# Optimization experiments

Measured on AMD Instinct MI355X. Metric: run time of the kernel, lower is better.

Reference implementation:

```python
import jax, jax.numpy as jnp
import numpy as np

B, S, D = 2, 2048, 1024
H, HD = 16, 64
MLP = 4096
EPS = 1e-5


def layer_norm(x, g, b):
    mu = jnp.mean(x, axis=-1, keepdims=True)
    var = jnp.mean(jnp.square(x - mu), axis=-1, keepdims=True)
    return (x - mu) * jax.lax.rsqrt(var + EPS) * g + b


def setup_inputs() -> dict:
    key = jax.random.key(0)
    ks = jax.random.split(key, 12)
    s = 0.02
    return {
        "x": jax.random.normal(ks[0], (B, S, D), jnp.float32),
        "ln1_g": jnp.ones((D,), jnp.float32),
        "ln1_b": jnp.zeros((D,), jnp.float32),
        "Wq": jax.random.normal(ks[1], (D, H * HD), jnp.float32) * s,
        "Wk": jax.random.normal(ks[2], (D, H * HD), jnp.float32) * s,
        "Wv": jax.random.normal(ks[3], (D, H * HD), jnp.float32) * s,
        "Wo": jax.random.normal(ks[4], (H * HD, D), jnp.float32) * s,
        "ln2_g": jnp.ones((D,), jnp.float32),
        "ln2_b": jnp.zeros((D,), jnp.float32),
        "fc1_w": jax.random.normal(ks[5], (D, MLP), jnp.float32) * s,
        "fc1_b": jnp.zeros((MLP,), jnp.float32),
        "fc2_w": jax.random.normal(ks[6], (MLP, D), jnp.float32) * s,
        "fc2_b": jnp.zeros((D,), jnp.float32),
    }


def reference(x, ln1_g, ln1_b, Wq, Wk, Wv, Wo, ln2_g, ln2_b, fc1_w, fc1_b, fc2_w, fc2_b):
    b, s, d = x.shape
    scale = 1.0 / np.sqrt(HD)
    h = layer_norm(x, ln1_g, ln1_b)
    # project and split heads: [b, H, s, HD]
    q = (h @ Wq).reshape(b, s, H, HD).transpose(0, 2, 1, 3)
    k = (h @ Wk).reshape(b, s, H, HD).transpose(0, 2, 1, 3)
    v = (h @ Wv).reshape(b, s, H, HD).transpose(0, 2, 1, 3)
    scores = jnp.einsum('bhqd,bhkd->bhqk', q, k) * scale
    causal = jnp.where(jnp.tril(jnp.ones((s, s), bool)), 0.0, -jnp.inf).astype(x.dtype)
    scores = scores + causal[None, None]
    attn_weights = jax.nn.softmax(scores, axis=-1)
    attn_out = jnp.einsum('bhqk,bhkd->bhqd', attn_weights, v)
    attn_out = attn_out.transpose(0, 2, 1, 3).reshape(b, s, H * HD) @ Wo
    x = x + attn_out
    h2 = layer_norm(x, ln2_g, ln2_b)
    mlp = jax.nn.gelu(h2 @ fc1_w + fc1_b, approximate=True) @ fc2_w + fc2_b
    x = x + mlp
    return (x, attn_weights)
```

## Files before the change

### kernel.cpp

```cpp
#include <hip/hip_runtime.h>
#include <cmath>

typedef __bf16 bf16;
typedef __bf16 bf16x8 __attribute__((ext_vector_type(8)));
typedef float f32x4 __attribute__((ext_vector_type(4)));

#define B_ 2
#define S_ 2048
#define D_ 1024
#define H_ 16
#define HD_ 64
#define MLP_ 4096
#define XOUT_ ((size_t)B_ * S_ * D_)

#define SBAR() __builtin_amdgcn_s_barrier()
#define VMCNT(N) asm volatile("s_waitcnt vmcnt(" #N ")" ::: "memory")
#define SFENCE() asm volatile("" ::: "memory")

__device__ __forceinline__ void gll16(const void* g, void* l) {
  __builtin_amdgcn_global_load_lds((const __attribute__((address_space(1))) void*)g,
                                   (__attribute__((address_space(3))) void*)l, 16, 0, 0);
}

__device__ __forceinline__ f32x4 mfma16(bf16x8 a, bf16x8 b, f32x4 c) {
  return __builtin_amdgcn_mfma_f32_16x16x32_bf16(a, b, c, 0, 0, 0);
}

__device__ __forceinline__ float bfu2f(unsigned short u) {
  return __uint_as_float(((unsigned int)u) << 16);
}
__device__ __forceinline__ unsigned short f2bu(float v) {
  union { bf16 b; unsigned short u; } c; c.b = (bf16)v; return c.u;
}
__device__ __forceinline__ float ld_sc(const void* p, size_t i, int f32) {
  return f32 ? ((const float*)p)[i] : bfu2f(((const unsigned short*)p)[i]);
}

__device__ __forceinline__ int swz(int row, int col) {
  int byo = row * 128 + col * 2;
  return (byo ^ (((byo >> 9) & 3) << 5)) >> 1;
}

__global__ __launch_bounds__(64) void detect_k(const unsigned short* __restrict__ x,
                                               int* __restrict__ flag) {
  int tid = threadIdx.x;
  int cnt = 0;
  for (int i = tid; i < 512; i += 64) {
    int e = (x[i] >> 7) & 0xFF;
    if (e >= 0xBF) cnt++;
  }
  #pragma unroll
  for (int d = 1; d < 64; d <<= 1) cnt += __shfl_xor(cnt, d);
  if (tid == 0) flag[0] = (cnt > 8) ? 1 : 0;
}

__global__ __launch_bounds__(256) void transpose_ad(const void* __restrict__ in,
                                                    unsigned short* __restrict__ out,
                                                    int R, int C,
                                                    const int* __restrict__ flagp) {
  __shared__ unsigned short t[64][68];
  const int f32 = flagp[0];
  const int tid = threadIdx.x;
  const int c0 = blockIdx.x * 64, r0 = blockIdx.y * 64;
  for (int i = tid * 4; i < 4096; i += 1024) {
    int rr = i >> 6, cc = i & 63;
    size_t off = (size_t)(r0 + rr) * C + c0 + cc;
    if (f32) {
      float4 f = *(const float4*)((const float*)in + off);
      t[rr][cc + 0] = f2bu(f.x); t[rr][cc + 1] = f2bu(f.y);
      t[rr][cc + 2] = f2bu(f.z); t[rr][cc + 3] = f2bu(f.w);
    } else {
      *(ushort4*)&t[rr][cc] = *(const ushort4*)((const unsigned short*)in + off);
    }
  }
  __syncthreads();
  for (int i = tid * 4; i < 4096; i += 1024) {
    int orr = i & 63, oc = i >> 6;
    ushort4 v;
    v.x = t[orr + 0][oc]; v.y = t[orr + 1][oc];
    v.z = t[orr + 2][oc]; v.w = t[orr + 3][oc];
    *(ushort4*)(out + (size_t)(c0 + oc) * R + r0 + orr) = v;
  }
}

__global__ __launch_bounds__(256) void vtrans_k(const unsigned short* __restrict__ qkv,
                                                unsigned short* __restrict__ vT) {
  __shared__ unsigned short t[64][68];
  const int tid = threadIdx.x;
  const int s0 = blockIdx.x * 64, h = blockIdx.y, b = blockIdx.z;
  for (int i = tid * 4; i < 4096; i += 1024) {
    int si = i >> 6, hd = i & 63;
    *(ushort4*)&t[si][hd] =
        *(const ushort4*)(qkv + (size_t)(b * S_ + s0 + si) * 3072 + 2048 + h * 64 + hd);
  }
  __syncthreads();
  for (int i = tid * 4; i < 4096; i += 1024) {
    int ss = i & 63, hd = i >> 6;
    ushort4 v;
    v.x = t[ss + 0][hd]; v.y = t[ss + 1][hd];
    v.z = t[ss + 2][hd]; v.w = t[ss + 3][hd];
    *(ushort4*)(vT + ((size_t)(b * H_ + h) * 64 + hd) * S_ + s0 + ss) = v;
  }
}

__global__ __launch_bounds__(256) void ln_k(const void* __restrict__ xv,
                                            const void* __restrict__ g,
                                            const void* __restrict__ bvec,
                                            bf16* __restrict__ out,
                                            const int* __restrict__ flagp,
                                            int force_xf32) {
  const int f32 = flagp[0];
  const int xf32 = force_xf32 ? 1 : f32;
  const int row = blockIdx.x, tid = threadIdx.x;
  float v[4];
  if (xf32) {
    float4 f = *(const float4*)((const float*)xv + (size_t)row * 1024 + tid * 4);
    v[0] = f.x; v[1] = f.y; v[2] = f.z; v[3] = f.w;
  } else {
    ushort4 u = *(const ushort4*)((const unsigned short*)xv + (size_t)row * 1024 + tid * 4);
    v[0] = bfu2f(u.x); v[1] = bfu2f(u.y); v[2] = bfu2f(u.z); v[3] = bfu2f(u.w);
  }
  float s = 0.f, q = 0.f;
  #pragma unroll
  for (int i = 0; i < 4; i++) { s += v[i]; q += v[i] * v[i]; }
  #pragma unroll
  for (int d = 1; d < 64; d <<= 1) { s += __shfl_xor(s, d); q += __shfl_xor(q, d); }
  __shared__ float red[8];
  if ((tid & 63) == 0) { red[(tid >> 6) * 2] = s; red[(tid >> 6) * 2 + 1] = q; }
  __syncthreads();
  s = red[0] + red[2] + red[4] + red[6];
  q = red[1] + red[3] + red[5] + red[7];
  const float mean = s * (1.0f / 1024.0f);
  const float var = q * (1.0f / 1024.0f) - mean * mean;
  const float rs = rsqrtf(var + 1e-5f);
  unsigned short ov[4];
  #pragma unroll
  for (int i = 0; i < 4; i++) {
    float gg = ld_sc(g, tid * 4 + i, f32);
    float bb = ld_sc(bvec, tid * 4 + i, f32);
    ov[i] = f2bu((v[i] - mean) * rs * gg + bb);
  }
  ushort4 o4; o4.x = ov[0]; o4.y = ov[1]; o4.z = ov[2]; o4.w = ov[3];
  *(ushort4*)((unsigned short*)out + (size_t)row * 1024 + tid * 4) = o4;
}

template <int MODE>
__global__ __launch_bounds__(256) void gemm_bt(const bf16* __restrict__ A,
                                               const bf16* __restrict__ BT,
                                               int N, int K,
                                               const void* __restrict__ bias,
                                               const void* __restrict__ resb,
                                               const float* __restrict__ resf,
                                               bf16* __restrict__ outb,
                                               float* __restrict__ outf,
                                               const int* __restrict__ flagp) {
  __shared__ __align__(16) bf16 sA[128 * 64];
  __shared__ __align__(16) bf16 sB[128 * 64];
  const int f32 = flagp[0];
  const int tid = threadIdx.x;
  const int lane = tid & 63;
  const int wave = tid >> 6;
  const int wm = wave >> 1, wn = wave & 1;
  const int m0 = blockIdx.y * 128, n0 = blockIdx.x * 128;
  const int cn = lane & 15, rl = lane >> 4;
  const int r0 = tid >> 3, c16 = tid & 7;

  f32x4 zero = {0.f, 0.f, 0.f, 0.f};
  f32x4 acc[4][4];
  #pragma unroll
  for (int i = 0; i < 4; i++)
    #pragma unroll
    for (int j = 0; j < 4; j++) acc[i][j] = zero;

  for (int k0 = 0; k0 < K; k0 += 64) {
    __syncthreads();
    #pragma unroll
    for (int i = 0; i < 4; i++) {
      int row = r0 + i * 32;
      gll16(A + (size_t)(m0 + row) * K + k0 + c16 * 8, &sA[row * 64 + c16 * 8]);
      gll16(BT + (size_t)(n0 + row) * K + k0 + c16 * 8, &sB[row * 64 + c16 * 8]);
    }
    __syncthreads();
    #pragma unroll
    for (int kk = 0; kk < 64; kk += 32) {
      bf16x8 af[4], bfr[4];
      #pragma unroll
      for (int t = 0; t < 4; t++) {
        af[t] = *(const bf16x8*)&sA[(wm * 64 + t * 16 + cn) * 64 + kk + rl * 8];
        bfr[t] = *(const bf16x8*)&sB[(wn * 64 + t * 16 + cn) * 64 + kk + rl * 8];
      }
      #pragma unroll
      for (int mt = 0; mt < 4; mt++)
        #pragma unroll
        for (int nt = 0; nt < 4; nt++)
          acc[mt][nt] = mfma16(af[mt], bfr[nt], acc[mt][nt]);
    }
  }

  #pragma unroll
  for (int mt = 0; mt < 4; mt++) {
    #pragma unroll
    for (int nt = 0; nt < 4; nt++) {
      #pragma unroll
      for (int j = 0; j < 4; j++) {
        const int row = m0 + wm * 64 + mt * 16 + rl * 4 + j;
        const int col = n0 + wn * 64 + nt * 16 + cn;
        const size_t idx = (size_t)row * N + col;
        float v = acc[mt][nt][j];
        if (MODE == 0) {
          outb[idx] = (bf16)v;
        } else if (MODE == 1) {
          v += ld_sc(bias, col, f32);
          float u = 0.7978845608028654f * (v + 0.044715f * v * v * v);
          float gl = v / (1.0f + exp2f(-2.8853900817779268f * u));
          outb[idx] = (bf16)gl;
        } else if (MODE == 2) {
          outf[idx] = v + ld_sc(resb, idx, f32);
        } else {
          float val = v + ld_sc(bias, col, f32) + resf[idx];
          if (f32) outf[idx] = val; else outb[idx] = (bf16)val;
        }
      }
    }
  }
}

__global__ __launch_bounds__(256) void attn_k(const bf16* __restrict__ qkv,
                                              const bf16* __restrict__ vT,
                                              void* __restrict__ Pv,
                                              bf16* __restrict__ ao,
                                              const int* __restrict__ flagp) {
  __shared__ __align__(16) bf16 sK[2][64 * 64];
  __shared__ __align__(16) bf16 sV[2][64 * 64];
  __shared__ __align__(16) bf16 sP[4][16 * 64];
  const int f32o = flagp[0];
  const int tid = threadIdx.x, lane = tid & 63, wave = tid >> 6;
  const int qt = (int)(gridDim.x - 1 - blockIdx.x);
  const int h = blockIdx.y, b = blockIdx.z;
  const float scale2 = 0.18033688011112042f;
  const float NEG = -1e30f;
  const int cn = lane & 15, rl = lane >> 4;

  int urow[2], ucol[2], ldst[2];
  #pragma unroll
  for (int i = 0; i < 2; i++) {
    int Lb = tid * 16 + i * 4096;
    int Ub = Lb ^ (((Lb >> 9) & 3) << 5);
    urow[i] = Ub >> 7;
    ucol[i] = (Ub & 127) >> 1;
    ldst[i] = Lb >> 1;
  }

  const bf16* kbase = qkv + (size_t)b * S_ * 3072 + 1024 + h * 64;
  const bf16* vbase = vT + ((size_t)(b * H_ + h) * 64) * S_;

  bf16x8 aq[2];
  {
    const bf16* qb = qkv + (size_t)(b * S_ + qt * 64 + wave * 16 + cn) * 3072 + h * 64;
    aq[0] = *(const bf16x8*)(qb + rl * 8);
    aq[1] = *(const bf16x8*)(qb + 32 + rl * 8);
  }

  #pragma unroll
  for (int i = 0; i < 2; i++)
    gll16(kbase + (size_t)urow[i] * 3072 + ucol[i], &sK[0][ldst[i]]);
  VMCNT(0);
  SBAR();

  float m_i[4], l_i[4];
  #pragma unroll
  for (int j = 0; j < 4; j++) { m_i[j] = NEG; l_i[j] = 0.0f; }

  int cur = 0;
  for (int kt = 0; kt <= qt; kt++) {
    if (kt < qt) {
      #pragma unroll
      for (int i = 0; i < 2; i++)
        gll16(kbase + (size_t)((kt + 1) * 64 + urow[i]) * 3072 + ucol[i], &sK[cur ^ 1][ldst[i]]);
      SFENCE();
    }
    f32x4 s[4];
    f32x4 zero = {0.f, 0.f, 0.f, 0.f};
    #pragma unroll
    for (int nt = 0; nt < 4; nt++) s[nt] = zero;
    #pragma unroll
    for (int kx = 0; kx < 2; kx++)
      #pragma unroll
      for (int nt = 0; nt < 4; nt++) {
        bf16x8 bb = *(const bf16x8*)&sK[cur][swz(nt * 16 + cn, kx * 32 + rl * 8)];
        s[nt] = mfma16(aq[kx], bb, s[nt]);
      }
    float pm[4] = {NEG, NEG, NEG, NEG};
    if (kt == qt) {
      #pragma unroll
      for (int nt = 0; nt < 4; nt++)
        #pragma unroll
        for (int j = 0; j < 4; j++) {
          float v = (nt * 16 + cn > wave * 16 + rl * 4 + j) ? NEG : s[nt][j] * scale2;
          s[nt][j] = v;
          pm[j] = fmaxf(pm[j], v);
        }
    } else {
      #pragma unroll
      for (int nt = 0; nt < 4; nt++)
        #pragma unroll
        for (int j = 0; j < 4; j++) {
          float v = s[nt][j] * scale2;
          s[nt][j] = v;
          pm[j] = fmaxf(pm[j], v);
        }
    }
    #pragma unroll
    for (int j = 0; j < 4; j++) {
      #pragma unroll
      for (int d = 1; d < 16; d <<= 1) pm[j] = fmaxf(pm[j], __shfl_xor(pm[j], d));
      float mn = fmaxf(m_i[j], pm[j]);
      float ps = exp2f(s[0][j] - mn) + exp2f(s[1][j] - mn) +
                 exp2f(s[2][j] - mn) + exp2f(s[3][j] - mn);
      #pragma unroll
      for (int d = 1; d < 16; d <<= 1) ps += __shfl_xor(ps, d);
      l_i[j] = l_i[j] * exp2f(m_i[j] - mn) + ps;
      m_i[j] = mn;
    }
    if (kt < qt) { VMCNT(0); SBAR(); cur ^= 1; }
  }

  float inv_l[4];
  #pragma unroll
  for (int j = 0; j < 4; j++) inv_l[j] = 1.0f / l_i[j];

  SBAR();
  #pragma unroll
  for (int i = 0; i < 2; i++) {
    gll16(kbase + (size_t)urow[i] * 3072 + ucol[i], &sK[0][ldst[i]]);
    gll16(vbase + (size_t)urow[i] * S_ + ucol[i], &sV[0][ldst[i]]);
  }
  VMCNT(0);
  SBAR();
  cur = 0;

  f32x4 o[4];
  {
    f32x4 zero = {0.f, 0.f, 0.f, 0.f};
    #pragma unroll
    for (int nt = 0; nt < 4; nt++) o[nt] = zero;
  }

  for (int kt = 0; kt <= qt; kt++) {
    if (kt < qt) {
      #pragma unroll
      for (int i = 0; i < 2; i++) {
        gll16(kbase + (size_t)((kt + 1) * 64 + urow[i]) * 3072 + ucol[i], &sK[cur ^ 1][ldst[i]]);
        gll16(vbase + (size_t)urow[i] * S_ + (kt + 1) * 64 + ucol[i], &sV[cur ^ 1][ldst[i]]);
      }
      SFENCE();
    }
    f32x4 s[4];
    f32x4 zero = {0.f, 0.f, 0.f, 0.f};
    #pragma unroll
    for (int nt = 0; nt < 4; nt++) s[nt] = zero;
    #pragma unroll
    for (int kx = 0; kx < 2; kx++)
      #pragma unroll
      for (int nt = 0; nt < 4; nt++) {
        bf16x8 bb = *(const bf16x8*)&sK[cur][swz(nt * 16 + cn, kx * 32 + rl * 8)];
        s[nt] = mfma16(aq[kx], bb, s[nt]);
      }
    if (kt == qt) {
      #pragma unroll
      for (int nt = 0; nt < 4; nt++)
        #pragma unroll
        for (int j = 0; j < 4; j++) {
          bool masked = (nt * 16 + cn > wave * 16 + rl * 4 + j);
          float p = masked ? 0.0f : exp2f(s[nt][j] * scale2 - m_i[j]) * inv_l[j];
          sP[wave][swz(rl * 4 + j, nt * 16 + cn)] = (bf16)p;
        }
    } else {
      #pragma unroll
      for (int nt = 0; nt < 4; nt++)
        #pragma unroll
        for (int j = 0; j < 4; j++) {
          float p = exp2f(s[nt][j] * scale2 - m_i[j]) * inv_l[j];
          sP[wave][swz(rl * 4 + j, nt * 16 + cn)] = (bf16)p;
        }
    }
    {
      size_t base = XOUT_ + (((size_t)b * H_ + h) * S_ + qt * 64 + wave * 16) * S_ + kt * 64;
      #pragma unroll
      for (int i = 0; i < 2; i++) {
        int idx = lane + i * 64;
        int r = idx >> 3, cc = idx & 7;
        uint4 val = *(const uint4*)&sP[wave][swz(r, cc * 8)];
        if (f32o) {
          float4 lo, hi;
          lo.x = __uint_as_float(val.x << 16); lo.y = __uint_as_float(val.x & 0xffff0000u);
          lo.z = __uint_as_float(val.y << 16); lo.w = __uint_as_float(val.y & 0xffff0000u);
          hi.x = __uint_as_float(val.z << 16); hi.y = __uint_as_float(val.z & 0xffff0000u);
          hi.z = __uint_as_float(val.w << 16); hi.w = __uint_as_float(val.w & 0xffff0000u);
          *(float4*)((float*)Pv + base + (size_t)r * S_ + cc * 8) = lo;
          *(float4*)((float*)Pv + base + (size_t)r * S_ + cc * 8 + 4) = hi;
        } else {
          *(uint4*)((bf16*)Pv + base + (size_t)r * S_ + cc * 8) = val;
        }
      }
    }
    #pragma unroll
    for (int kx = 0; kx < 2; kx++) {
      bf16x8 ap = *(const bf16x8*)&sP[wave][swz(cn, kx * 32 + rl * 8)];
      #pragma unroll
      for (int nt = 0; nt < 4; nt++) {
        bf16x8 bv = *(const bf16x8*)&sV[cur][swz(nt * 16 + cn, kx * 32 + rl * 8)];
        o[nt] = mfma16(ap, bv, o[nt]);
      }
    }
    if (kt < qt) {
      if (f32o) { VMCNT(4); } else { VMCNT(2); }
      SBAR();
      cur ^= 1;
    }
  }

  {
    const int t0 = qt + 1;
    const int nch = (32 - t0) * 8;
    size_t rowbase = XOUT_ + (((size_t)b * H_ + h) * S_ + qt * 64) * S_;
    uint4 z; z.x = 0; z.y = 0; z.z = 0; z.w = 0;
    for (int idx = tid; idx < 64 * nch; idx += 256) {
      int r = idx / nch, cc = idx % nch;
      size_t off = rowbase + (size_t)r * S_ + t0 * 64 + cc * 8;
      if (f32o) {
        *(uint4*)((float*)Pv + off) = z;
        *(uint4*)((float*)Pv + off + 4) = z;
      } else {
        *(uint4*)((bf16*)Pv + off) = z;
      }
    }
  }

  #pragma unroll
  for (int nt = 0; nt < 4; nt++)
    #pragma unroll
    for (int j = 0; j < 4; j++) {
      int rowg2 = b * S_ + qt * 64 + wave * 16 + rl * 4 + j;
      ao[(size_t)rowg2 * 1024 + h * 64 + nt * 16 + cn] = (bf16)o[nt][j];
    }
}

extern "C" void kernel_launch(void* const* d_in, const int* in_sizes, int n_in,
                              void* d_out, int out_size, void* d_ws, size_t ws_size,
                              hipStream_t stream) {
  (void)in_sizes; (void)n_in; (void)out_size; (void)ws_size;
  const void* x    = d_in[0];
  const void* ln1g = d_in[1];
  const void* ln1b = d_in[2];
  const void* Wq   = d_in[3];
  const void* Wk   = d_in[4];
  const void* Wv   = d_in[5];
  const void* Wo   = d_in[6];
  const void* ln2g = d_in[7];
  const void* ln2b = d_in[8];
  const void* fc1w = d_in[9];
  const void* fc1b = d_in[10];
  const void* fc2w = d_in[11];
  const void* fc2b = d_in[12];

  char* ws = (char*)d_ws;
  bf16* wqkvT = (bf16*)(ws + 0);
  bf16* woT   = (bf16*)(ws + 6291456);
  bf16* fc1T  = (bf16*)(ws + 8388608);
  bf16* fc2T  = (bf16*)(ws + 16777216);
  bf16* h     = (bf16*)(ws + 25165824);
  bf16* qkv   = (bf16*)(ws + 33554432);
  bf16* vT    = (bf16*)(ws + 58720256);
  bf16* m1    = (bf16*)(ws + 33554432);
  bf16* aout  = (bf16*)(ws + 67108864);
  float* x1   = (float*)(ws + 75497472);
  int* flag   = (int*)(ws + 92274688);

  dim3 blk(256);

  detect_k<<<1, 64, 0, stream>>>((const unsigned short*)x, flag);

  transpose_ad<<<dim3(16, 16), blk, 0, stream>>>(Wq, (unsigned short*)wqkvT, 1024, 1024, flag);
  transpose_ad<<<dim3(16, 16), blk, 0, stream>>>(Wk, (unsigned short*)(wqkvT + 1024 * 1024), 1024, 1024, flag);
  transpose_ad<<<dim3(16, 16), blk, 0, stream>>>(Wv, (unsigned short*)(wqkvT + 2 * 1024 * 1024), 1024, 1024, flag);
  transpose_ad<<<dim3(16, 16), blk, 0, stream>>>(Wo, (unsigned short*)woT, 1024, 1024, flag);
  transpose_ad<<<dim3(64, 16), blk, 0, stream>>>(fc1w, (unsigned short*)fc1T, 1024, 4096, flag);
  transpose_ad<<<dim3(16, 64), blk, 0, stream>>>(fc2w, (unsigned short*)fc2T, 4096, 1024, flag);

  ln_k<<<4096, blk, 0, stream>>>(x, ln1g, ln1b, h, flag, 0);

  gemm_bt<0><<<dim3(24, 32), blk, 0, stream>>>(h, wqkvT, 3072, 1024, nullptr, nullptr, nullptr, qkv, nullptr, flag);

  vtrans_k<<<dim3(32, 16, 2), blk, 0, stream>>>((const unsigned short*)qkv, (unsigned short*)vT);

  attn_k<<<dim3(32, 16, 2), blk, 0, stream>>>(qkv, vT, d_out, aout, flag);

  gemm_bt<2><<<dim3(8, 32), blk, 0, stream>>>(aout, woT, 1024, 1024, nullptr, x, nullptr, nullptr, x1, flag);

  ln_k<<<4096, blk, 0, stream>>>(x1, ln2g, ln2b, h, flag, 1);

  gemm_bt<1><<<dim3(32, 32), blk, 0, stream>>>(h, fc1T, 4096, 1024, fc1b, nullptr, nullptr, m1, nullptr, flag);

  gemm_bt<3><<<dim3(8, 32), blk, 0, stream>>>(m1, fc2T, 1024, 4096, fc2b, nullptr, x1, (bf16*)d_out, (float*)d_out, flag);
}
```

Baseline: 1.075 ms.

## Add 128x64 GEMM tiles, XCD-aware block remap, deeper attention prefetch, fused weight transposes

Merges the four square weight transposes into one launch. Adds a block-ID remap in the GEMMs and the attention kernel so that consecutive workgroups, which land on different XCDs, share tiles within each XCD's L2. Adds a 128x64-tile GEMM for the N=1024 output projection and fc2 so those launches have twice as many workgroups. In the attention statistics pass it prefetches K two tiles ahead and defers the cross-lane max/sum reductions to the end of the loop. This raises occupancy and cache locality but adds index arithmetic and reduces reuse per tile in the narrower GEMM.

```diff
diff --git a/kernel.cpp b/kernel.cpp
--- a/kernel.cpp
+++ b/kernel.cpp
@@ -83,6 +83,41 @@
   }
 }
 
+__global__ __launch_bounds__(256) void transpose4_ad(const void* __restrict__ i0,
+                                                     const void* __restrict__ i1,
+                                                     const void* __restrict__ i2,
+                                                     const void* __restrict__ i3,
+                                                     unsigned short* __restrict__ wqkvT,
+                                                     unsigned short* __restrict__ woT,
+                                                     const int* __restrict__ flagp) {
+  __shared__ unsigned short t[64][68];
+  const int f32 = flagp[0];
+  const int tid = threadIdx.x;
+  const int z = blockIdx.z;
+  const void* in = (z == 0) ? i0 : (z == 1) ? i1 : (z == 2) ? i2 : i3;
+  unsigned short* out = (z < 3) ? (wqkvT + (size_t)z * 1024 * 1024) : woT;
+  const int c0 = blockIdx.x * 64, r0 = blockIdx.y * 64;
+  for (int i = tid * 4; i < 4096; i += 1024) {
+    int rr = i >> 6, cc = i & 63;
+    size_t off = (size_t)(r0 + rr) * 1024 + c0 + cc;
+    if (f32) {
+      float4 f = *(const float4*)((const float*)in + off);
+      t[rr][cc + 0] = f2bu(f.x); t[rr][cc + 1] = f2bu(f.y);
+      t[rr][cc + 2] = f2bu(f.z); t[rr][cc + 3] = f2bu(f.w);
+    } else {
+      *(ushort4*)&t[rr][cc] = *(const ushort4*)((const unsigned short*)in + off);
+    }
+  }
+  __syncthreads();
+  for (int i = tid * 4; i < 4096; i += 1024) {
+    int orr = i & 63, oc = i >> 6;
+    ushort4 v;
+    v.x = t[orr + 0][oc]; v.y = t[orr + 1][oc];
+    v.z = t[orr + 2][oc]; v.w = t[orr + 3][oc];
+    *(ushort4*)(out + (size_t)(c0 + oc) * 1024 + r0 + orr) = v;
+  }
+}
+
 __global__ __launch_bounds__(256) void vtrans_k(const unsigned short* __restrict__ qkv,
                                                 unsigned short* __restrict__ vT) {
   __shared__ unsigned short t[64][68];
@@ -161,7 +196,10 @@
   const int lane = tid & 63;
   const int wave = tid >> 6;
   const int wm = wave >> 1, wn = wave & 1;
-  const int m0 = blockIdx.y * 128, n0 = blockIdx.x * 128;
+  const int nwg = gridDim.x * gridDim.y;
+  const int fid = blockIdx.y * gridDim.x + blockIdx.x;
+  const int wg = ((nwg & 7) == 0) ? ((fid & 7) * (nwg >> 3) + (fid >> 3)) : fid;
+  const int m0 = (wg / gridDim.x) * 128, n0 = (wg % gridDim.x) * 128;
   const int cn = lane & 15, rl = lane >> 4;
   const int r0 = tid >> 3, c16 = tid & 7;
 
@@ -225,18 +263,101 @@
   }
 }
 
+template <int MODE>
+__global__ __launch_bounds__(256) void gemm_n64(const bf16* __restrict__ A,
+                                                const bf16* __restrict__ BT,
+                                                int N, int K,
+                                                const void* __restrict__ bias,
+                                                const void* __restrict__ resb,
+                                                const float* __restrict__ resf,
+                                                bf16* __restrict__ outb,
+                                                float* __restrict__ outf,
+                                                const int* __restrict__ flagp) {
+  __shared__ __align__(16) bf16 sA[128 * 64];
+  __shared__ __align__(16) bf16 sB[64 * 64];
+  const int f32 = flagp[0];
+  const int tid = threadIdx.x;
+  const int lane = tid & 63;
+  const int wave = tid >> 6;
+  const int nwg = gridDim.x * gridDim.y;
+  const int fid = blockIdx.y * gridDim.x + blockIdx.x;
+  const int wg = ((nwg & 7) == 0) ? ((fid & 7) * (nwg >> 3) + (fid >> 3)) : fid;
+  const int m0 = (wg / gridDim.x) * 128, n0 = (wg % gridDim.x) * 64;
+  const int cn = lane & 15, rl = lane >> 4;
+  const int r0 = tid >> 3, c16 = tid & 7;
+
+  f32x4 zero = {0.f, 0.f, 0.f, 0.f};
+  f32x4 acc[2][4];
+  #pragma unroll
+  for (int i = 0; i < 2; i++)
+    #pragma unroll
+    for (int j = 0; j < 4; j++) acc[i][j] = zero;
+
+  for (int k0 = 0; k0 < K; k0 += 64) {
+    __syncthreads();
+    #pragma unroll
+    for (int i = 0; i < 4; i++) {
+      int row = r0 + i * 32;
+      gll16(A + (size_t)(m0 + row) * K + k0 + c16 * 8, &sA[row * 64 + c16 * 8]);
+    }
+    #pragma unroll
+    for (int i = 0; i < 2; i++) {
+      int row = r0 + i * 32;
+      gll16(BT + (size_t)(n0 + row) * K + k0 + c16 * 8, &sB[row * 64 + c16 * 8]);
+    }
+    __syncthreads();
+    #pragma unroll
+    for (int kk = 0; kk < 64; kk += 32) {
+      bf16x8 af[2], bfr[4];
+      #pragma unroll
+      for (int t = 0; t < 2; t++)
+        af[t] = *(const bf16x8*)&sA[(wave * 32 + t * 16 + cn) * 64 + kk + rl * 8];
+      #pragma unroll
+      for (int t = 0; t < 4; t++)
+        bfr[t] = *(const bf16x8*)&sB[(t * 16 + cn) * 64 + kk + rl * 8];
+      #pragma unroll
+      for (int mt = 0; mt < 2; mt++)
+        #pragma unroll
+        for (int nt = 0; nt < 4; nt++)
+          acc[mt][nt] = mfma16(af[mt], bfr[nt], acc[mt][nt]);
+    }
+  }
+
+  #pragma unroll
+  for (int mt = 0; mt < 2; mt++) {
+    #pragma unroll
+    for (int nt = 0; nt < 4; nt++) {
+      #pragma unroll
+      for (int j = 0; j < 4; j++) {
+        const int row = m0 + wave * 32 + mt * 16 + rl * 4 + j;
+        const int col = n0 + nt * 16 + cn;
+        const size_t idx = (size_t)row * N + col;
+        float v = acc[mt][nt][j];
+        if (MODE == 2) {
+          outf[idx] = v + ld_sc(resb, idx, f32);
+        } else {
+          float val = v + ld_sc(bias, col, f32) + resf[idx];
+          if (f32) outf[idx] = val; else outb[idx] = (bf16)val;
+        }
+      }
+    }
+  }
+}
+
 __global__ __launch_bounds__(256) void attn_k(const bf16* __restrict__ qkv,
                                               const bf16* __restrict__ vT,
                                               void* __restrict__ Pv,
                                               bf16* __restrict__ ao,
                                               const int* __restrict__ flagp) {
-  __shared__ __align__(16) bf16 sK[2][64 * 64];
-  __shared__ __align__(16) bf16 sV[2][64 * 64];
+  __shared__ __align__(16) bf16 sKV[4][64 * 64];
   __shared__ __align__(16) bf16 sP[4][16 * 64];
   const int f32o = flagp[0];
   const int tid = threadIdx.x, lane = tid & 63, wave = tid >> 6;
-  const int qt = (int)(gridDim.x - 1 - blockIdx.x);
-  const int h = blockIdx.y, b = blockIdx.z;
+  const int fid = blockIdx.x;
+  const int c8 = fid & 7, kk8 = fid >> 3;
+  const int qt = 31 - (kk8 & 31);
+  const int p = c8 + 8 * (kk8 >> 5);
+  const int h = p & 15, b = p >> 4;
   const float scale2 = 0.18033688011112042f;
   const float NEG = -1e30f;
   const int cn = lane & 15, rl = lane >> 4;
@@ -261,83 +382,84 @@
     aq[1] = *(const bf16x8*)(qb + 32 + rl * 8);
   }
 
-  #pragma unroll
-  for (int i = 0; i < 2; i++)
-    gll16(kbase + (size_t)urow[i] * 3072 + ucol[i], &sK[0][ldst[i]]);
+#define STAGEK(kt_, s_) { \
+    _Pragma("unroll") for (int i = 0; i < 2; i++) \
+      gll16(kbase + (size_t)((kt_) * 64 + urow[i]) * 3072 + ucol[i], &sKV[s_][ldst[i]]); }
+#define STAGEV(kt_, s_) { \
+    _Pragma("unroll") for (int i = 0; i < 2; i++) \
+      gll16(vbase + (size_t)urow[i] * S_ + (kt_) * 64 + ucol[i], &sKV[s_][ldst[i]]); }
+
+  float m_i[4], l_i[4];
+  #pragma unroll
+  for (int j = 0; j < 4; j++) { m_i[j] = NEG; l_i[j] = 0.0f; }
+
+  STAGEK(0, 0);
+  if (qt >= 1) { STAGEK(1, 1); SFENCE(); VMCNT(2); } else { VMCNT(0); }
+  SBAR();
+
+  for (int kt = 0; kt <= qt; kt++) {
+    if (kt + 2 <= qt) { STAGEK(kt + 2, ((kt + 2) & 3)); SFENCE(); }
+    const int slot = kt & 3;
+    f32x4 s4[4];
+    f32x4 zero = {0.f, 0.f, 0.f, 0.f};
+    #pragma unroll
+    for (int nt = 0; nt < 4; nt++) s4[nt] = zero;
+    #pragma unroll
+    for (int kx = 0; kx < 2; kx++)
+      #pragma unroll
+      for (int nt = 0; nt < 4; nt++) {
+        bf16x8 bb = *(const bf16x8*)&sKV[slot][swz(nt * 16 + cn, kx * 32 + rl * 8)];
+        s4[nt] = mfma16(aq[kx], bb, s4[nt]);
+      }
+    if (kt == qt) {
+      #pragma unroll
+      for (int nt = 0; nt < 4; nt++)
+        #pragma unroll
+        for (int j = 0; j < 4; j++)
+          s4[nt][j] = (nt * 16 + cn > wave * 16 + rl * 4 + j) ? NEG : s4[nt][j] * scale2;
+    } else {
+      #pragma unroll
+      for (int nt = 0; nt < 4; nt++)
+        #pragma unroll
+        for (int j = 0; j < 4; j++) s4[nt][j] *= scale2;
+    }
+    #pragma unroll
+    for (int j = 0; j < 4; j++) {
+      float pm = fmaxf(fmaxf(s4[0][j], s4[1][j]), fmaxf(s4[2][j], s4[3][j]));
+      float mn = fmaxf(m_i[j], pm);
+      float ps = exp2f(s4[0][j] - mn) + exp2f(s4[1][j] - mn) +
+                 exp2f(s4[2][j] - mn) + exp2f(s4[3][j] - mn);
+      l_i[j] = l_i[j] * exp2f(m_i[j] - mn) + ps;
+      m_i[j] = mn;
+    }
+    if (kt < qt) {
+      if (kt + 2 <= qt) { VMCNT(2); } else { VMCNT(0); }
+      SBAR();
+    }
+  }
+
+  #pragma unroll
+  for (int j = 0; j < 4; j++) {
+    float mr = m_i[j];
+    #pragma unroll
+    for (int d = 1; d < 16; d <<= 1) mr = fmaxf(mr, __shfl_xor(mr, d));
+    float lr = l_i[j] * exp2f(m_i[j] - mr);
+    #pragma unroll
+    for (int d = 1; d < 16; d <<= 1) lr += __shfl_xor(lr, d);
+    m_i[j] = mr;
+    l_i[j] = lr;
+  }
+
+  float inv_l[4];
+  #pragma unroll
+  for (int j = 0; j < 4; j++) inv_l[j] = 1.0f / l_i[j];
+
+  SBAR();
+  STAGEK(0, 0);
+  STAGEV(0, 2);
   VMCNT(0);
   SBAR();
-
-  float m_i[4], l_i[4];
-  #pragma unroll
-  for (int j = 0; j < 4; j++) { m_i[j] = NEG; l_i[j] = 0.0f; }
-
   int cur = 0;
-  for (int kt = 0; kt <= qt; kt++) {
-    if (kt < qt) {
-      #pragma unroll
-      for (int i = 0; i < 2; i++)
-        gll16(kbase + (size_t)((kt + 1) * 64 + urow[i]) * 3072 + ucol[i], &sK[cur ^ 1][ldst[i]]);
-      SFENCE();
-    }
-    f32x4 s[4];
-    f32x4 zero = {0.f, 0.f, 0.f, 0.f};
-    #pragma unroll
-    for (int nt = 0; nt < 4; nt++) s[nt] = zero;
-    #pragma unroll
-    for (int kx = 0; kx < 2; kx++)
-      #pragma unroll
-      for (int nt = 0; nt < 4; nt++) {
-        bf16x8 bb = *(const bf16x8*)&sK[cur][swz(nt * 16 + cn, kx * 32 + rl * 8)];
-        s[nt] = mfma16(aq[kx], bb, s[nt]);
-      }
-    float pm[4] = {NEG, NEG, NEG, NEG};
-    if (kt == qt) {
-      #pragma unroll
-      for (int nt = 0; nt < 4; nt++)
-        #pragma unroll
-        for (int j = 0; j < 4; j++) {
-          float v = (nt * 16 + cn > wave * 16 + rl * 4 + j) ? NEG : s[nt][j] * scale2;
-          s[nt][j] = v;
-          pm[j] = fmaxf(pm[j], v);
-        }
-    } else {
-      #pragma unroll
-      for (int nt = 0; nt < 4; nt++)
-        #pragma unroll
-        for (int j = 0; j < 4; j++) {
-          float v = s[nt][j] * scale2;
-          s[nt][j] = v;
-          pm[j] = fmaxf(pm[j], v);
-        }
-    }
-    #pragma unroll
-    for (int j = 0; j < 4; j++) {
-      #pragma unroll
-      for (int d = 1; d < 16; d <<= 1) pm[j] = fmaxf(pm[j], __shfl_xor(pm[j], d));
-      float mn = fmaxf(m_i[j], pm[j]);
-      float ps = exp2f(s[0][j] - mn) + exp2f(s[1][j] - mn) +
-                 exp2f(s[2][j] - mn) + exp2f(s[3][j] - mn);
-      #pragma unroll
-      for (int d = 1; d < 16; d <<= 1) ps += __shfl_xor(ps, d);
-      l_i[j] = l_i[j] * exp2f(m_i[j] - mn) + ps;
-      m_i[j] = mn;
-    }
-    if (kt < qt) { VMCNT(0); SBAR(); cur ^= 1; }
-  }
-
-  float inv_l[4];
-  #pragma unroll
-  for (int j = 0; j < 4; j++) inv_l[j] = 1.0f / l_i[j];
-
-  SBAR();
-  #pragma unroll
-  for (int i = 0; i < 2; i++) {
-    gll16(kbase + (size_t)urow[i] * 3072 + ucol[i], &sK[0][ldst[i]]);
-    gll16(vbase + (size_t)urow[i] * S_ + ucol[i], &sV[0][ldst[i]]);
-  }
-  VMCNT(0);
-  SBAR();
-  cur = 0;
 
   f32x4 o[4];
   {
@@ -348,23 +470,20 @@
 
   for (int kt = 0; kt <= qt; kt++) {
     if (kt < qt) {
-      #pragma unroll
-      for (int i = 0; i < 2; i++) {
-        gll16(kbase + (size_t)((kt + 1) * 64 + urow[i]) * 3072 + ucol[i], &sK[cur ^ 1][ldst[i]]);
-        gll16(vbase + (size_t)urow[i] * S_ + (kt + 1) * 64 + ucol[i], &sV[cur ^ 1][ldst[i]]);
-      }
+      STAGEK(kt + 1, (cur ^ 1));
+      STAGEV(kt + 1, (2 + (cur ^ 1)));
       SFENCE();
     }
-    f32x4 s[4];
+    f32x4 s4[4];
     f32x4 zero = {0.f, 0.f, 0.f, 0.f};
     #pragma unroll
-    for (int nt = 0; nt < 4; nt++) s[nt] = zero;
+    for (int nt = 0; nt < 4; nt++) s4[nt] = zero;
     #pragma unroll
     for (int kx = 0; kx < 2; kx++)
       #pragma unroll
       for (int nt = 0; nt < 4; nt++) {
-        bf16x8 bb = *(const bf16x8*)&sK[cur][swz(nt * 16 + cn, kx * 32 + rl * 8)];
-        s[nt] = mfma16(aq[kx], bb, s[nt]);
+        bf16x8 bb = *(const bf16x8*)&sKV[cur][swz(nt * 16 + cn, kx * 32 + rl * 8)];
+        s4[nt] = mfma16(aq[kx], bb, s4[nt]);
       }
     if (kt == qt) {
       #pragma unroll
@@ -372,16 +491,16 @@
         #pragma unroll
         for (int j = 0; j < 4; j++) {
           bool masked = (nt * 16 + cn > wave * 16 + rl * 4 + j);
-          float p = masked ? 0.0f : exp2f(s[nt][j] * scale2 - m_i[j]) * inv_l[j];
-          sP[wave][swz(rl * 4 + j, nt * 16 + cn)] = (bf16)p;
+          float pv = masked ? 0.0f : exp2f(s4[nt][j] * scale2 - m_i[j]) * inv_l[j];
+          sP[wave][swz(rl * 4 + j, nt * 16 + cn)] = (bf16)pv;
         }
     } else {
       #pragma unroll
       for (int nt = 0; nt < 4; nt++)
         #pragma unroll
         for (int j = 0; j < 4; j++) {
-          float p = exp2f(s[nt][j] * scale2 - m_i[j]) * inv_l[j];
-          sP[wave][swz(rl * 4 + j, nt * 16 + cn)] = (bf16)p;
+          float pv = exp2f(s4[nt][j] * scale2 - m_i[j]) * inv_l[j];
+          sP[wave][swz(rl * 4 + j, nt * 16 + cn)] = (bf16)pv;
         }
     }
     {
@@ -409,7 +528,7 @@
       bf16x8 ap = *(const bf16x8*)&sP[wave][swz(cn, kx * 32 + rl * 8)];
       #pragma unroll
       for (int nt = 0; nt < 4; nt++) {
-        bf16x8 bv = *(const bf16x8*)&sV[cur][swz(nt * 16 + cn, kx * 32 + rl * 8)];
+        bf16x8 bv = *(const bf16x8*)&sKV[2 + cur][swz(nt * 16 + cn, kx * 32 + rl * 8)];
         o[nt] = mfma16(ap, bv, o[nt]);
       }
     }
@@ -444,6 +563,8 @@
       int rowg2 = b * S_ + qt * 64 + wave * 16 + rl * 4 + j;
       ao[(size_t)rowg2 * 1024 + h * 64 + nt * 16 + cn] = (bf16)o[nt][j];
     }
+#undef STAGEK
+#undef STAGEV
 }
 
 extern "C" void kernel_launch(void* const* d_in, const int* in_sizes, int n_in,
@@ -481,10 +602,8 @@
 
   detect_k<<<1, 64, 0, stream>>>((const unsigned short*)x, flag);
 
-  transpose_ad<<<dim3(16, 16), blk, 0, stream>>>(Wq, (unsigned short*)wqkvT, 1024, 1024, flag);
-  transpose_ad<<<dim3(16, 16), blk, 0, stream>>>(Wk, (unsigned short*)(wqkvT + 1024 * 1024), 1024, 1024, flag);
-  transpose_ad<<<dim3(16, 16), blk, 0, stream>>>(Wv, (unsigned short*)(wqkvT + 2 * 1024 * 1024), 1024, 1024, flag);
-  transpose_ad<<<dim3(16, 16), blk, 0, stream>>>(Wo, (unsigned short*)woT, 1024, 1024, flag);
+  transpose4_ad<<<dim3(16, 16, 4), blk, 0, stream>>>(Wq, Wk, Wv, Wo,
+      (unsigned short*)wqkvT, (unsigned short*)woT, flag);
   transpose_ad<<<dim3(64, 16), blk, 0, stream>>>(fc1w, (unsigned short*)fc1T, 1024, 4096, flag);
   transpose_ad<<<dim3(16, 64), blk, 0, stream>>>(fc2w, (unsigned short*)fc2T, 4096, 1024, flag);
 
@@ -494,13 +613,13 @@
 
   vtrans_k<<<dim3(32, 16, 2), blk, 0, stream>>>((const unsigned short*)qkv, (unsigned short*)vT);
 
-  attn_k<<<dim3(32, 16, 2), blk, 0, stream>>>(qkv, vT, d_out, aout, flag);
-
-  gemm_bt<2><<<dim3(8, 32), blk, 0, stream>>>(aout, woT, 1024, 1024, nullptr, x, nullptr, nullptr, x1, flag);
+  attn_k<<<dim3(1024), blk, 0, stream>>>(qkv, vT, d_out, aout, flag);
+
+  gemm_n64<2><<<dim3(16, 32), blk, 0, stream>>>(aout, woT, 1024, 1024, nullptr, x, nullptr, nullptr, x1, flag);
 
   ln_k<<<4096, blk, 0, stream>>>(x1, ln2g, ln2b, h, flag, 1);
 
   gemm_bt<1><<<dim3(32, 32), blk, 0, stream>>>(h, fc1T, 4096, 1024, fc1b, nullptr, nullptr, m1, nullptr, flag);
 
-  gemm_bt<3><<<dim3(8, 32), blk, 0, stream>>>(m1, fc2T, 1024, 4096, fc2b, nullptr, x1, (bf16*)d_out, (float*)d_out, flag);
-}
+  gemm_n64<3><<<dim3(16, 32), blk, 0, stream>>>(m1, fc2T, 1024, 4096, fc2b, nullptr, x1, (bf16*)d_out, (float*)d_out, flag);
+}
```

Measured after the change: 979.1 us. 8.9% less time.
